# Performance work log

Measured on AMD Instinct MI355X. Metric: run time of the kernel, lower is better.

## Reference

```python
import jax, jax.numpy as jnp
import numpy as np

EPS = 1e-8
LN_EPS = 1e-5

def _ln(x, g, b):
    m = x.mean(-1, keepdims=True)
    v = ((x - m) ** 2).mean(-1, keepdims=True)
    return (x - m) * jax.lax.rsqrt(v + LN_EPS) * g + b

def _rbf(d, n_rbf):
    # standard protein RBF embedding: gaussians on [0, 20] Angstrom
    mu = jnp.linspace(0.0, 20.0, n_rbf)
    sigma = 20.0 / n_rbf
    return jnp.exp(-(((d[..., None] - mu) / sigma) ** 2))

def setup_inputs() -> dict:
    N, K, CS, CZ, G, RBF = 1024, 16, 256, 128, 16, 64
    key = jax.random.key(0)
    ks = jax.random.split(key, 24)
    s = 0.02
    inp = {
        'node_features': jax.random.normal(ks[0], (N, CS), jnp.float32),
        'trans': jax.random.normal(ks[1], (N, 3), jnp.float32) * 10.0,
        'src_edge_features': jax.random.normal(ks[2], (N, K, CZ), jnp.float32),
        'dst_edge_features': jax.random.normal(ks[3], (N, K, CZ), jnp.float32),
        # params
        'ln_src_g': jnp.ones((CZ,)), 'ln_src_b': jnp.zeros((CZ,)),
        'ln_dst_g': jnp.ones((CZ,)), 'ln_dst_b': jnp.zeros((CZ,)),
        'W_nl': jax.random.normal(ks[4], (G, CS)) * s, 'b_nl': jnp.zeros((G,)),
        'W_nr': jax.random.normal(ks[5], (G, CS)) * s, 'b_nr': jnp.zeros((G,)),
        'W_ep': jax.random.normal(ks[6], (CZ, CZ)) * s, 'b_ep': jnp.zeros((CZ,)),
        'W_eg': jax.random.normal(ks[7], (CZ, CZ)) * s, 'b_eg': jnp.zeros((CZ,)),
        'W_dg': jax.random.normal(ks[8], (CZ, G, G)) * s, 'b_dg': jnp.zeros((CZ,)),
        'W_dp': jax.random.normal(ks[9], (CZ, RBF)) * s, 'b_dp': jnp.zeros((CZ,)),
        'ln_out_g': jnp.ones((CZ,)), 'ln_out_b': jnp.zeros((CZ,)),
        'W_lo': jax.random.normal(ks[10], (CZ, CZ)) * s, 'b_lo': jnp.zeros((CZ,)),
        'W_og': jax.random.normal(ks[11], (CZ, CZ)) * s, 'b_og': jnp.zeros((CZ,)),
        # int / mask args (KNN form)
        'src_edge_index': jax.random.randint(ks[12], (2, N, K), 0, N, jnp.int32),
        'dst_edge_index': jax.random.randint(ks[13], (2, N, K), 0, N, jnp.int32),
        'src_mask': jnp.ones((N, K), bool),
        'dst_mask': jnp.ones((N, K), bool),
    }
    return inp

def reference(node_features, trans, src_edge_features, dst_edge_features,
              ln_src_g, ln_src_b, ln_dst_g, ln_dst_b,
              W_nl, b_nl, W_nr, b_nr, W_ep, b_ep, W_eg, b_eg,
              W_dg, b_dg, W_dp, b_dp, ln_out_g, ln_out_b,
              W_lo, b_lo, W_og, b_og,
              src_edge_index, dst_edge_index, src_mask, dst_mask):
    N, K, CZ = src_edge_features.shape
    src_ln = _ln(src_edge_features, ln_src_g, ln_src_b)   # [N,K,CZ]
    dst_ln = _ln(dst_edge_features, ln_dst_g, ln_dst_b)
    node_left = node_features @ W_nl.T + b_nl              # [N,G]
    node_right = node_features @ W_nr.T + b_nr
    e1 = node_left[src_edge_index[0]]                      # [N,K,G]
    e2 = node_right[dst_edge_index[0]]                     # [N,K,G]
    # triangle gate: fuse outer product [N,K,K,G,G] with dist_gate Linear
    t = jnp.einsum('nia,zab->nizb', e1, W_dg)
    gate3 = jnp.einsum('nizb,njb->nijz', t, e2) + b_dg     # [N,K,K,CZ]
    t1 = trans[src_edge_index[0]]                          # [N,K,3]
    t2 = trans[dst_edge_index[0]]
    d = jnp.linalg.norm(t1[:, :, None, :] - t2[:, None, :, :] + EPS, axis=-1)  # [N,K,K]
    distf = _rbf(d, W_dp.shape[1]) @ W_dp.T + b_dp         # [N,K,K,CZ]
    mask3 = (src_mask[:, :, None] & dst_mask[:, None, :])[..., None]
    edge3 = jax.nn.sigmoid(gate3) * distf * mask3          # [N,K,K,CZ]
    edge2 = jax.nn.sigmoid(src_ln @ W_eg.T + b_eg) * (src_ln @ W_ep.T + b_ep)  # [N,K,CZ]
    # batched per-channel combine: sum over dst slot j
    upd = jnp.einsum('nijz,njz->niz', edge3, edge2)        # [N,K,CZ]
    upd = _ln(upd, ln_out_g, ln_out_b) @ W_lo.T + b_lo
    upd = upd * jax.nn.sigmoid(dst_ln @ W_og.T + b_og)
    upd = upd * dst_mask[..., None]                        # knn -> sparse (masked flatten)
    return upd.reshape(N * K, CZ)
```

## Files before the change

kernel.cpp:

```cpp
#include <hip/hip_runtime.h>
#include <hip/hip_bf16.h>
#include <stdint.h>

#define N_    1024
#define K_    16
#define CZ_   128
#define G_    16
#define RBF_  64
#define CS_   256

typedef const float* fp;
typedef _Float16 f16x8 __attribute__((ext_vector_type(8)));
typedef _Float16 h2    __attribute__((ext_vector_type(2)));
typedef float f32x4    __attribute__((ext_vector_type(4)));

#define MFMA16(A,B,C) __builtin_amdgcn_mfma_f32_16x16x32_f16(A,B,C,0,0,0)

#define OFF_EGH 0
#define OFF_EPH 16384
#define OFF_OGH 32768
#define OFF_LOH 49152
#define OFF_DPH 65536
#define OFF_DGT 73728

__device__ __forceinline__ float sigm(float x){
  return __builtin_amdgcn_rcpf(1.0f + __expf(-x));
}
__device__ __forceinline__ unsigned short f2h(float v){
  union{_Float16 h; unsigned short u;} c; c.h = (_Float16)v; return c.u;
}
__device__ __forceinline__ float h2f(unsigned short u){
  union{unsigned short u; _Float16 h;} c; c.u = u; return (float)c.h;
}
__device__ __forceinline__ unsigned int pk2(float a, float b){
  union{h2 h; unsigned int u;} c; c.h[0] = (_Float16)a; c.h[1] = (_Float16)b; return c.u;
}
__device__ __forceinline__ f16x8 ldh8(const unsigned short* p){
  union{uint4 u; f16x8 h;} c; c.u = *(const uint4*)p; return c.h;
}
__device__ __forceinline__ f16x8 ldh8u(const unsigned short* p){
  union{uint2 u[2]; f16x8 h;} c;
  c.u[0] = *(const uint2*)p;
  c.u[1] = *(const uint2*)(p+4);
  return c.h;
}
__device__ __forceinline__ f16x8 cvt8(float4 a, float4 b){
  f16x8 r;
  r[0]=(_Float16)a.x; r[1]=(_Float16)a.y; r[2]=(_Float16)a.z; r[3]=(_Float16)a.w;
  r[4]=(_Float16)b.x; r[5]=(_Float16)b.y; r[6]=(_Float16)b.z; r[7]=(_Float16)b.w;
  return r;
}

__global__ __launch_bounds__(256) void repack(
    fp W_eg, fp W_ep, fp W_og, fp W_lo, fp W_dp, fp W_dg,
    unsigned short* __restrict__ ws)
{
  int t = blockIdx.x*256 + threadIdx.x;
  int stride = gridDim.x*256;
  for (int i = t; i < 16384; i += stride) {
    ws[OFF_EGH+i] = f2h(W_eg[i]);
    ws[OFF_EPH+i] = f2h(W_ep[i]);
    ws[OFF_OGH+i] = f2h(W_og[i]);
    ws[OFF_LOH+i] = f2h(W_lo[i]);
  }
  for (int i = t; i < 8192; i += stride)
    ws[OFF_DPH+i] = f2h(W_dp[i]);
  for (int i = t; i < 32768; i += stride) {
    int z = i >> 8, rem = i & 255, b = rem >> 4, a = rem & 15;
    ws[OFF_DGT+i] = f2h(W_dg[z*256 + a*16 + b]);
  }
}

__global__ __launch_bounds__(512, 4) void tri_fused6(
    fp nf, fp trans, fp srcef, fp dstef,
    fp ln_src_g, fp ln_src_b, fp ln_dst_g, fp ln_dst_b,
    fp W_nl, fp b_nl, fp W_nr, fp b_nr,
    fp b_eg, fp b_ep, fp b_og,
    fp b_dg, fp b_dp, fp ln_out_g, fp ln_out_b, fp b_lo,
    const int* __restrict__ sidx, const int* __restrict__ didx,
    const unsigned short* __restrict__ ws,
    float* __restrict__ out)
{
  __shared__ __align__(16) float updf[K_*132];
  __shared__ __align__(16) unsigned short bufB[2*K_*136];
  __shared__ __align__(16) unsigned short rbfH[4*64*20];
  __shared__ __align__(16) unsigned short edge2h[128*18];
  __shared__ __align__(16) unsigned short sogh[16*128];
  __shared__ __align__(16) unsigned short e1h[16*16];
  __shared__ __align__(16) unsigned short e2h[16*18];
  __shared__ __align__(16) float t1f[16][4];
  __shared__ __align__(16) float t2f[16][4];

  unsigned short* srcH = bufB;
  unsigned short* dstH = bufB + 2176;
  unsigned short* updH = bufB;

  const int n   = blockIdx.x;
  const int tid = threadIdx.x;
  const int wv  = tid >> 6;
  const int lnn = tid & 63;
  const int lm  = lnn & 15;
  const int lq  = lnn >> 4;

  if (tid < 32) {
    int k = tid & 15;
    int id2 = (tid < 16) ? sidx[n*K_ + k] : didx[n*K_ + k];
    float* tf = (tid < 16) ? &t1f[k][0] : &t2f[k][0];
    tf[0] = trans[id2*3+0]; tf[1] = trans[id2*3+1]; tf[2] = trans[id2*3+2];
  }
  {
    int row = tid >> 4;
    int c0  = (tid & 15) * 8;
    int r16 = row & 15;
    bool isSrc = row < 16;
    const float* base = (isSrc ? srcef : dstef) + (n*K_ + r16)*CZ_ + c0;
    float4 xa = *(const float4*)base;
    float4 xb = *(const float4*)(base+4);
    float x[8] = {xa.x,xa.y,xa.z,xa.w,xb.x,xb.y,xb.z,xb.w};
    float s = x[0]+x[1]+x[2]+x[3]+x[4]+x[5]+x[6]+x[7];
    s += __shfl_xor(s,1); s += __shfl_xor(s,2);
    s += __shfl_xor(s,4); s += __shfl_xor(s,8);
    float m = s * 0.0078125f;
    float q = 0.f;
    #pragma unroll
    for (int i = 0; i < 8; ++i) { float d = x[i]-m; q += d*d; }
    q += __shfl_xor(q,1); q += __shfl_xor(q,2);
    q += __shfl_xor(q,4); q += __shfl_xor(q,8);
    float rv = rsqrtf(q * 0.0078125f + 1e-5f);
    fp gp = isSrc ? ln_src_g : ln_dst_g;
    fp bp = isSrc ? ln_src_b : ln_dst_b;
    float y[8];
    #pragma unroll
    for (int i = 0; i < 8; ++i) y[i] = (x[i]-m)*rv*gp[c0+i] + bp[c0+i];
    uint4 uh;
    uh.x = pk2(y[0],y[1]); uh.y = pk2(y[2],y[3]); uh.z = pk2(y[4],y[5]); uh.w = pk2(y[6],y[7]);
    *(uint4*)&((isSrc ? srcH : dstH)[r16*136 + c0]) = uh;
  }
  __syncthreads();

  {
    const int which = wv & 1;
    const int h     = wv >> 1;
    int idx = (which ? didx : sidx)[n*K_ + lm];
    const float* arow = nf + idx*CS_;
    const float* wrow = (which ? W_nr : W_nl) + lm*CS_;
    f32x4 acc = {0.f,0.f,0.f,0.f};
    #pragma unroll
    for (int kk = 0; kk < 2; ++kk) {
      int kb = h*64 + kk*32;
      f16x8 ah = cvt8(*(const float4*)(arow + kb + lq*8),
                      *(const float4*)(arow + kb + lq*8 + 4));
      f16x8 bh = cvt8(*(const float4*)(wrow + kb + lq*8),
                      *(const float4*)(wrow + kb + lq*8 + 4));
      acc = MFMA16(ah, bh, acc);
    }
    float* pst = (float*)updf;
    #pragma unroll
    for (int r = 0; r < 4; ++r)
      pst[wv*256 + r*64 + lnn] = acc[r];
  }

  {
    const int z = wv*16 + lm;
    f32x4 aeg = {0.f,0.f,0.f,0.f}, aep = {0.f,0.f,0.f,0.f}, aog = {0.f,0.f,0.f,0.f};
    #pragma unroll
    for (int kb = 0; kb < 128; kb += 32) {
      f16x8 sh = ldh8(srcH + lm*136 + kb + lq*8);
      f16x8 dh = ldh8(dstH + lm*136 + kb + lq*8);
      f16x8 wegv = ldh8(ws + OFF_EGH + z*128 + kb + lq*8);
      f16x8 weph = ldh8(ws + OFF_EPH + z*128 + kb + lq*8);
      f16x8 wogv = ldh8(ws + OFF_OGH + z*128 + kb + lq*8);
      aeg = MFMA16(sh, wegv, aeg);
      aep = MFMA16(sh, weph, aep);
      aog = MFMA16(dh, wogv, aog);
    }
    float beg = b_eg[z], bep = b_ep[z], bog = b_og[z];
    #pragma unroll
    for (int r = 0; r < 4; ++r) {
      int j = lq*4 + r;
      edge2h[z*18 + j] = f2h(sigm(aeg[r]+beg) * (aep[r]+bep));
      sogh[j*128 + z]  = f2h(sigm(aog[r]+bog));
    }
  }
  __syncthreads();

  if (wv < 2) {
    const float* pst = (const float*)updf;
    float bias = (wv ? b_nr : b_nl)[lm];
    #pragma unroll
    for (int r = 0; r < 4; ++r) {
      float v = pst[(wv  )*256 + r*64 + lnn]
              + pst[(wv+2)*256 + r*64 + lnn]
              + pst[(wv+4)*256 + r*64 + lnn]
              + pst[(wv+6)*256 + r*64 + lnn];
      v += bias;
      if (wv) e2h[(lq*4+r)*18 + lm] = f2h(v);
      else    e1h[(lq*4+r)*16 + lm] = f2h(v);
    }
  }
  __syncthreads();

  {
    const int z = wv*16 + lm;
    f16x8 Bdg[8];
    #pragma unroll
    for (int q = 0; q < 8; ++q)
      Bdg[q] = ldh8(ws + OFF_DGT + z*256 + q*32 + lq*8);
    f16x8 Bdp0 = ldh8(ws + OFF_DPH + z*64 + lq*8);
    f16x8 Bdp1 = ldh8(ws + OFF_DPH + z*64 + 32 + lq*8);
    const float bdg = b_dg[z], bdp = b_dp[z];
    const float inv_sigma = 3.2f;
    const float mustep = 20.0f/63.0f;
    _Float16 e2s[8];
    #pragma unroll
    for (int q = 0; q < 8; ++q) {
      union{unsigned short u; _Float16 hh;} c;
      c.u = e2h[lm*18 + 2*q + (lq>>1)];
      e2s[q] = c.hh;
    }
    float e2v4[4];
    #pragma unroll
    for (int r = 0; r < 4; ++r) e2v4[r] = h2f(edge2h[z*18 + lq*4 + r]);

    for (int qt = 0; qt < 4; ++qt) {
      __syncthreads();
      {
        int slot = wv & 3;
        int i  = qt*4 + slot;
        int kh = wv >> 2;
        float dx = t1f[i][0]-t2f[lm][0]+1e-8f;
        float dy = t1f[i][1]-t2f[lm][1]+1e-8f;
        float dz = t1f[i][2]-t2f[lm][2]+1e-8f;
        float d = sqrtf(dx*dx+dy*dy+dz*dz);
        union { f16x8 hh; uint2 u2[2]; } cv;
        #pragma unroll
        for (int c = 0; c < 8; ++c) {
          int k = kh*32 + lq*8 + c;
          float t = (d - (float)k*mustep) * inv_sigma;
          cv.hh[c] = (_Float16)__expf(-t*t);
        }
        unsigned short* dp = &rbfH[(slot*64+lnn)*20 + kh*8];
        *(uint2*)dp     = cv.u2[0];
        *(uint2*)(dp+4) = cv.u2[1];
      }
      __syncthreads();
      for (int ii = 0; ii < 4; ++ii) {
        int i = qt*4 + ii;
        f16x8 e1v = ldh8(e1h + i*16 + (lq&1)*8);
        f32x4 accg = {0.f,0.f,0.f,0.f};
        #pragma unroll
        for (int q = 0; q < 8; ++q) {
          f16x8 av;
          _Float16 sc = e2s[q];
          #pragma unroll
          for (int c = 0; c < 8; ++c) av[c] = e1v[c] * sc;
          accg = MFMA16(av, Bdg[q], accg);
        }
        const unsigned short* rp = &rbfH[(ii*64+lnn)*20];
        f16x8 r0 = ldh8u(rp);
        f16x8 r1 = ldh8u(rp + 8);
        f32x4 accp = {0.f,0.f,0.f,0.f};
        accp = MFMA16(r0, Bdp0, accp);
        accp = MFMA16(r1, Bdp1, accp);
        float s = 0.f;
        #pragma unroll
        for (int r = 0; r < 4; ++r)
          s += sigm(accg[r]+bdg) * (accp[r]+bdp) * e2v4[r];
        s += __shfl_xor(s,16); s += __shfl_xor(s,32);
        if (lq == 0) updf[i*132 + z] = s;
      }
    }
  }
  __syncthreads();

  {
    int row = tid >> 5;
    int c0  = (tid & 31) * 4;
    float4 x = *(const float4*)&updf[row*132 + c0];
    float s = x.x+x.y+x.z+x.w;
    s += __shfl_xor(s,1,32); s += __shfl_xor(s,2,32); s += __shfl_xor(s,4,32);
    s += __shfl_xor(s,8,32); s += __shfl_xor(s,16,32);
    float m = s * 0.0078125f;
    float q = (x.x-m)*(x.x-m)+(x.y-m)*(x.y-m)+(x.z-m)*(x.z-m)+(x.w-m)*(x.w-m);
    q += __shfl_xor(q,1,32); q += __shfl_xor(q,2,32); q += __shfl_xor(q,4,32);
    q += __shfl_xor(q,8,32); q += __shfl_xor(q,16,32);
    float rv = rsqrtf(q*0.0078125f + 1e-5f);
    float y0 = (x.x-m)*rv*ln_out_g[c0+0] + ln_out_b[c0+0];
    float y1 = (x.y-m)*rv*ln_out_g[c0+1] + ln_out_b[c0+1];
    float y2 = (x.z-m)*rv*ln_out_g[c0+2] + ln_out_b[c0+2];
    float y3 = (x.w-m)*rv*ln_out_g[c0+3] + ln_out_b[c0+3];
    uint2 uh;
    uh.x = pk2(y0,y1); uh.y = pk2(y2,y3);
    *(uint2*)&updH[row*136 + c0] = uh;
  }
  __syncthreads();

  {
    const int z = wv*16 + lm;
    f32x4 acc = {0.f,0.f,0.f,0.f};
    #pragma unroll
    for (int kb = 0; kb < 128; kb += 32) {
      f16x8 ah = ldh8(updH + lm*136 + kb + lq*8);
      f16x8 bh = ldh8(ws + OFF_LOH + z*128 + kb + lq*8);
      acc = MFMA16(ah, bh, acc);
    }
    float blo = b_lo[z];
    #pragma unroll
    for (int r = 0; r < 4; ++r) {
      int islot = lq*4 + r;
      out[(n*K_ + islot)*CZ_ + z] = (acc[r] + blo) * h2f(sogh[islot*128 + z]);
    }
  }
}

extern "C" void kernel_launch(void* const* d_in, const int* in_sizes, int n_in,
                              void* d_out, int out_size, void* d_ws, size_t ws_size,
                              hipStream_t stream)
{
  fp nodef    = (fp)d_in[0];
  fp trans    = (fp)d_in[1];
  fp srcef    = (fp)d_in[2];
  fp dstef    = (fp)d_in[3];
  fp ln_src_g = (fp)d_in[4];  fp ln_src_b = (fp)d_in[5];
  fp ln_dst_g = (fp)d_in[6];  fp ln_dst_b = (fp)d_in[7];
  fp W_nl = (fp)d_in[8];   fp b_nl = (fp)d_in[9];
  fp W_nr = (fp)d_in[10];  fp b_nr = (fp)d_in[11];
  fp W_ep = (fp)d_in[12];  fp b_ep = (fp)d_in[13];
  fp W_eg = (fp)d_in[14];  fp b_eg = (fp)d_in[15];
  fp W_dg = (fp)d_in[16];  fp b_dg = (fp)d_in[17];
  fp W_dp = (fp)d_in[18];  fp b_dp = (fp)d_in[19];
  fp ln_out_g = (fp)d_in[20]; fp ln_out_b = (fp)d_in[21];
  fp W_lo = (fp)d_in[22];  fp b_lo = (fp)d_in[23];
  fp W_og = (fp)d_in[24];  fp b_og = (fp)d_in[25];
  const int* sidx = (const int*)d_in[26];
  const int* didx = (const int*)d_in[27];

  unsigned short* ws16 = (unsigned short*)d_ws;
  float* outp = (float*)d_out;

  hipLaunchKernelGGL(repack, dim3(64), dim3(256), 0, stream,
                     W_eg, W_ep, W_og, W_lo, W_dp, W_dg, ws16);
  hipLaunchKernelGGL(tri_fused6, dim3(N_), dim3(512), 0, stream,
                     nodef, trans, srcef, dstef,
                     ln_src_g, ln_src_b, ln_dst_g, ln_dst_b,
                     W_nl, b_nl, W_nr, b_nr,
                     b_eg, b_ep, b_og,
                     b_dg, b_dp, ln_out_g, ln_out_b, b_lo,
                     sidx, didx, ws16, outp);
}
```

Before: 179.6 us.

## Factor triangle gate into two-stage MFMA via LDS intermediate t

The triangle gate was computed as a rank-1 outer-product times W_dg using eight MFMAs per row i, with the f16 operand rebuilt by elementwise scaling each time. It is now split into two stages. First t = e1·W_dg is computed per output channel with MFMA and stored as f16 in LDS. Then, for each i, a single MFMA contracts e2 with t. W_dg is repacked into a new layout for the first stage, and shared memory becomes one manually carved pool with larger intermediates, processed in two halves of eight rows. This cuts MFMA and VALU work and frees the registers that held Bdg, at the cost of more LDS traffic, extra f16 rounding of t, and higher LDS use that may reduce occupancy.

```diff
diff --git a/kernel.cpp b/kernel.cpp
--- a/kernel.cpp
+++ b/kernel.cpp
@@ -21,7 +21,7 @@
 #define OFF_OGH 32768
 #define OFF_LOH 49152
 #define OFF_DPH 65536
-#define OFF_DGT 73728
+#define OFF_DGA 73728
 
 __device__ __forceinline__ float sigm(float x){
   return __builtin_amdgcn_rcpf(1.0f + __expf(-x));
@@ -66,8 +66,11 @@
   for (int i = t; i < 8192; i += stride)
     ws[OFF_DPH+i] = f2h(W_dp[i]);
   for (int i = t; i < 32768; i += stride) {
-    int z = i >> 8, rem = i & 255, b = rem >> 4, a = rem & 15;
-    ws[OFF_DGT+i] = f2h(W_dg[z*256 + a*16 + b]);
+    int z = i >> 8, rem = i & 255;
+    int l = rem >> 3, c = rem & 7;
+    int a = ((l >> 4) << 3) | c;
+    int b = l & 15;
+    ws[OFF_DGA+i] = f2h(W_dg[z*256 + a*16 + b]);
   }
 }
 
@@ -81,19 +84,20 @@
     const unsigned short* __restrict__ ws,
     float* __restrict__ out)
 {
-  __shared__ __align__(16) float updf[K_*132];
-  __shared__ __align__(16) unsigned short bufB[2*K_*136];
-  __shared__ __align__(16) unsigned short rbfH[4*64*20];
-  __shared__ __align__(16) unsigned short edge2h[128*18];
-  __shared__ __align__(16) unsigned short sogh[16*128];
-  __shared__ __align__(16) unsigned short e1h[16*16];
-  __shared__ __align__(16) unsigned short e2h[16*18];
-  __shared__ __align__(16) float t1f[16][4];
-  __shared__ __align__(16) float t2f[16][4];
-
-  unsigned short* srcH = bufB;
-  unsigned short* dstH = bufB + 2176;
-  unsigned short* updH = bufB;
+  __shared__ __align__(16) unsigned char smem[72192];
+  float*          updf   = (float*)smem;
+  unsigned short* edge2h = (unsigned short*)(smem + 8448);
+  unsigned short* sogh   = (unsigned short*)(smem + 13056);
+  unsigned short* e1h    = (unsigned short*)(smem + 17152);
+  unsigned short* e2h    = (unsigned short*)(smem + 17664);
+  float (*t1f)[4]        = (float(*)[4])(smem + 18304);
+  float (*t2f)[4]        = (float(*)[4])(smem + 18560);
+  unsigned short* poolH  = (unsigned short*)(smem + 18816);
+  unsigned short* srcH   = poolH;
+  unsigned short* dstH   = poolH + 2176;
+  unsigned short* t_lds  = poolH;
+  unsigned short* rbfH   = poolH + 16448;
+  unsigned short* updH   = poolH;
 
   const int n   = blockIdx.x;
   const int tid = threadIdx.x;
@@ -194,7 +198,7 @@
               + pst[(wv+4)*256 + r*64 + lnn]
               + pst[(wv+6)*256 + r*64 + lnn];
       v += bias;
-      if (wv) e2h[(lq*4+r)*18 + lm] = f2h(v);
+      if (wv) e2h[(lq*4+r)*20 + lm] = f2h(v);
       else    e1h[(lq*4+r)*16 + lm] = f2h(v);
     }
   }
@@ -202,60 +206,68 @@
 
   {
     const int z = wv*16 + lm;
-    f16x8 Bdg[8];
-    #pragma unroll
-    for (int q = 0; q < 8; ++q)
-      Bdg[q] = ldh8(ws + OFF_DGT + z*256 + q*32 + lq*8);
     f16x8 Bdp0 = ldh8(ws + OFF_DPH + z*64 + lq*8);
     f16x8 Bdp1 = ldh8(ws + OFF_DPH + z*64 + 32 + lq*8);
     const float bdg = b_dg[z], bdp = b_dp[z];
+    float e2v4[4];
+    #pragma unroll
+    for (int r = 0; r < 4; ++r) e2v4[r] = h2f(edge2h[z*18 + lq*4 + r]);
+
+    f16x8 zf = {(_Float16)0,(_Float16)0,(_Float16)0,(_Float16)0,
+                (_Float16)0,(_Float16)0,(_Float16)0,(_Float16)0};
+    f16x8 e1B = zf;
+    f16x8 e2A = zf;
+    if (lq < 2) {
+      e1B = ldh8 (e1h + lm*16 + lq*8);
+      e2A = ldh8u(e2h + lm*20 + lq*8);
+    }
     const float inv_sigma = 3.2f;
     const float mustep = 20.0f/63.0f;
-    _Float16 e2s[8];
-    #pragma unroll
-    for (int q = 0; q < 8; ++q) {
-      union{unsigned short u; _Float16 hh;} c;
-      c.u = e2h[lm*18 + 2*q + (lq>>1)];
-      e2s[q] = c.hh;
-    }
-    float e2v4[4];
-    #pragma unroll
-    for (int r = 0; r < 4; ++r) e2v4[r] = h2f(edge2h[z*18 + lq*4 + r]);
-
-    for (int qt = 0; qt < 4; ++qt) {
+
+    for (int h = 0; h < 2; ++h) {
       __syncthreads();
+      for (int zz = 0; zz < 16; ++zz) {
+        int za = wv*16 + zz;
+        f16x8 Ad = zf;
+        if (lnn < 32) Ad = ldh8(ws + OFF_DGA + za*256 + lnn*8);
+        f32x4 d4 = MFMA16(Ad, e1B, ((f32x4){0.f,0.f,0.f,0.f}));
+        if ((lm >> 3) == h) {
+          int ii = lm & 7;
+          uint2 u;
+          u.x = pk2(d4[0], d4[1]);
+          u.y = pk2(d4[2], d4[3]);
+          *(uint2*)&t_lds[ii*2056 + za*16 + lq*4] = u;
+        }
+      }
       {
-        int slot = wv & 3;
-        int i  = qt*4 + slot;
-        int kh = wv >> 2;
-        float dx = t1f[i][0]-t2f[lm][0]+1e-8f;
-        float dy = t1f[i][1]-t2f[lm][1]+1e-8f;
-        float dz = t1f[i][2]-t2f[lm][2]+1e-8f;
-        float d = sqrtf(dx*dx+dy*dy+dz*dz);
-        union { f16x8 hh; uint2 u2[2]; } cv;
+        const int kh = wv & 1;
         #pragma unroll
-        for (int c = 0; c < 8; ++c) {
-          int k = kh*32 + lq*8 + c;
-          float t = (d - (float)k*mustep) * inv_sigma;
-          cv.hh[c] = (_Float16)__expf(-t*t);
+        for (int p = 0; p < 2; ++p) {
+          int slot = (wv >> 1) + p*4;
+          int i = h*8 + slot;
+          float dx = t1f[i][0]-t2f[lm][0]+1e-8f;
+          float dy = t1f[i][1]-t2f[lm][1]+1e-8f;
+          float dz = t1f[i][2]-t2f[lm][2]+1e-8f;
+          float d = sqrtf(dx*dx+dy*dy+dz*dz);
+          union { f16x8 hh; uint2 u2[2]; } cv;
+          #pragma unroll
+          for (int c = 0; c < 8; ++c) {
+            int k = kh*32 + lq*8 + c;
+            float tt = (d - (float)k*mustep) * inv_sigma;
+            cv.hh[c] = (_Float16)__expf(-tt*tt);
+          }
+          unsigned short* dp = &rbfH[(slot*64+lnn)*20 + kh*8];
+          *(uint2*)dp     = cv.u2[0];
+          *(uint2*)(dp+4) = cv.u2[1];
         }
-        unsigned short* dp = &rbfH[(slot*64+lnn)*20 + kh*8];
-        *(uint2*)dp     = cv.u2[0];
-        *(uint2*)(dp+4) = cv.u2[1];
       }
       __syncthreads();
-      for (int ii = 0; ii < 4; ++ii) {
-        int i = qt*4 + ii;
-        f16x8 e1v = ldh8(e1h + i*16 + (lq&1)*8);
-        f32x4 accg = {0.f,0.f,0.f,0.f};
-        #pragma unroll
-        for (int q = 0; q < 8; ++q) {
-          f16x8 av;
-          _Float16 sc = e2s[q];
-          #pragma unroll
-          for (int c = 0; c < 8; ++c) av[c] = e1v[c] * sc;
-          accg = MFMA16(av, Bdg[q], accg);
-        }
+
+      for (int ii = 0; ii < 8; ++ii) {
+        int i = h*8 + ii;
+        f16x8 tB = zf;
+        if (lq < 2) tB = ldh8(t_lds + ii*2056 + z*16 + lq*8);
+        f32x4 accg = MFMA16(e2A, tB, ((f32x4){0.f,0.f,0.f,0.f}));
         const unsigned short* rp = &rbfH[(ii*64+lnn)*20];
         f16x8 r0 = ldh8u(rp);
         f16x8 r1 = ldh8u(rp + 8);
```

Result: no change. 181.2 us (+0.9%).
